# Optimization experiments

Hardware: AMD Instinct MI355X
Metric: run time of the kernel (lower is better)

The kernel has to match this reference:

```python
import jax, jax.numpy as jnp
import numpy as np
from jax import lax

EPS = 1e-08


def setup_inputs() -> dict:
    key = jax.random.key(0)
    k1, k2, k3 = jax.random.split(key, 3)
    b, cin, cout, ks, h, w = 16, 64, 64, 3, 256, 256
    X = jax.random.normal(k1, (b, cin, h, w), dtype=jnp.float32)
    y = jax.random.normal(k2, (b, cin), dtype=jnp.float32)
    weight = jax.random.normal(k3, (cout, cin, ks, ks), dtype=jnp.float32)
    return {"X": X, "y": y, "weight": weight}


def reference(X, y, weight):
    # EqualizedWeight: scale by Kaiming constant c = (cin*k*k)^-0.5 (gain=lr_mul=1)
    cout, cin, ks, _ = weight.shape
    c = (cin * ks * ks) ** (-0.5)
    w0 = weight * c
    # Modulate: per-sample, per-input-channel scaling -> (b, cout, cin, k, k)
    w1 = w0[None] * y[:, None, :, None, None]
    # Demodulate: normalize each (sample, out-filter) to unit L2 norm
    d = lax.rsqrt(jnp.sum(w1 * w1, axis=(2, 3, 4), keepdims=True) + EPS)
    w1 = w1 * d
    b, _, h, w = X.shape
    # Grouped conv: fold batch into channels, one group per sample
    Xr = X.reshape(1, b * cin, h, w)
    ker = w1.reshape(b * cout, cin, ks, ks)
    out = lax.conv_general_dilated(
        Xr, ker,
        window_strides=(1, 1),
        padding="SAME",
        feature_group_count=b,
        dimension_numbers=("NCHW", "OIHW", "NCHW"),
    )
    return out.reshape(b, cout, h, w)
```

## Files before the change

kernel.cpp:

```cpp
#include <hip/hip_runtime.h>
#include <hip/hip_bf16.h>

typedef __bf16 bf16x8 __attribute__((ext_vector_type(8)));
typedef float  f32x4  __attribute__((ext_vector_type(4)));

#define B_   16
#define CIN  64
#define COUT 64
#define H_   256
#define W_   256
#define TY   16
#define SLOT (258 * 64)

__global__ void modw_kernel(const float* __restrict__ weight,
                            const float* __restrict__ y,
                            __bf16* __restrict__ w1g) {
  const int co = blockIdx.x;
  const int b  = blockIdx.y;
  const int ci = threadIdx.x;
  const float c  = 0.041666666666666664f;
  const float yv = y[b*CIN + ci] * c;
  float w[9];
  float s = 0.0f;
#pragma unroll
  for (int t = 0; t < 9; ++t) {
    float wv = weight[(co*CIN + ci)*9 + t] * yv;
    w[t] = wv;
    s += wv * wv;
  }
#pragma unroll
  for (int off = 32; off > 0; off >>= 1) s += __shfl_xor(s, off, 64);
  const float d = rsqrtf(s + 1e-8f);
#pragma unroll
  for (int t = 0; t < 9; ++t)
    w1g[((b*9 + t)*COUT + co)*CIN + ci] = (__bf16)(w[t] * d);
}

__device__ __forceinline__ void stage_load(const float* __restrict__ X,
                                           int b, int yy, int tid, float4* f) {
  const int cg = tid >> 6;
  const int px_base = 4 * (tid & 63);
  const float* xrow = X + ((long)b * (CIN * H_ * W_) + (long)yy * W_);
#pragma unroll
  for (int j = 0; j < 8; ++j)
    f[j] = *reinterpret_cast<const float4*>(xrow + (long)(cg * 8 + j) * (H_ * W_) + px_base);
}

__device__ __forceinline__ void stage_write(__bf16* __restrict__ xs, int slot,
                                            int tid, const float4* f, bool valid) {
  const int cg = tid >> 6;
  const int px_base = 4 * (tid & 63);
  bf16x8 frag[4];
  if (valid) {
#pragma unroll
    for (int j = 0; j < 8; ++j) {
      frag[0][j] = (__bf16)f[j].x;
      frag[1][j] = (__bf16)f[j].y;
      frag[2][j] = (__bf16)f[j].z;
      frag[3][j] = (__bf16)f[j].w;
    }
  } else {
#pragma unroll
    for (int o = 0; o < 4; ++o)
#pragma unroll
      for (int j = 0; j < 8; ++j) frag[o][j] = (__bf16)0.f;
  }
#pragma unroll
  for (int oo = 0; oo < 4; ++oo) {
    const int o  = (oo + tid) & 3;
    const int pl = px_base + o + 1;
    const int gs = cg ^ (pl & 7);
    *reinterpret_cast<bf16x8*>(&xs[slot * SLOT + pl * 64 + gs * 8]) = frag[o];
  }
}

__global__ __launch_bounds__(512)
void conv_kernel(const float* __restrict__ X,
                 const __bf16* __restrict__ w1g,
                 float* __restrict__ out) {
  const int y0   = blockIdx.x * TY;
  const int b    = blockIdx.y;
  const int tid  = threadIdx.x;
  const int lane = tid & 63;
  const int wv   = tid >> 6;
  const int cgw  = wv & 1;
  const int pg   = wv >> 1;
  const int q    = lane >> 4;
  const int n    = lane & 15;

  __shared__ __bf16 xs[3 * SLOT];

  if (tid < 384) {
    const int s = tid >> 7, r = tid & 127;
    const int col = (r < 64) ? 0 : 257;
    xs[s * SLOT + col * 64 + (r & 63)] = (__bf16)0.f;
  }

  {
    float4 f[8];
#pragma unroll
    for (int k = 0; k < 3; ++k) {
      const int yy = y0 - 1 + k;
      const bool valid = (yy >= 0);
      if (valid) stage_load(X, b, yy, tid, f);
      stage_write(xs, (yy + 3) % 3, tid, f, valid);
    }
  }

  float4 pf[8];
  for (int ty = 0; ty < TY; ++ty) {
    const int y = y0 + ty;
    __syncthreads();

    const int yy = y + 2;
    const bool do_pf = (ty < TY - 1);
    const bool pf_ok = do_pf && (yy < H_);
    if (pf_ok) stage_load(X, b, yy, tid, pf);

    f32x4 acc[2][4];
#pragma unroll
    for (int c2 = 0; c2 < 2; ++c2)
#pragma unroll
      for (int nt = 0; nt < 4; ++nt) acc[c2][nt] = (f32x4){0.f, 0.f, 0.f, 0.f};

#pragma unroll
    for (int dy = 0; dy < 3; ++dy) {
      const __bf16* sl = &xs[((y - 1 + dy + 3) % 3) * SLOT];

      bf16x8 afr[2][3][2];
#pragma unroll
      for (int c2 = 0; c2 < 2; ++c2) {
        const int co = cgw * 32 + c2 * 16 + n;
#pragma unroll
        for (int dx = 0; dx < 3; ++dx) {
          const int tap = dy * 3 + dx;
          const __bf16* wp = w1g + ((b * 9 + tap) * COUT + co) * CIN + q * 8;
          afr[c2][dx][0] = *reinterpret_cast<const bf16x8*>(wp);
          afr[c2][dx][1] = *reinterpret_cast<const bf16x8*>(wp + 32);
        }
      }

#pragma unroll
      for (int dx = 0; dx < 3; ++dx) {
        const int p3 = (n + dx) & 7;
        const int o0 = (q ^ p3) * 8;
        const int o1 = ((q + 4) ^ p3) * 8;
#pragma unroll
        for (int nt = 0; nt < 4; ++nt) {
          const int px = pg * 64 + nt * 16 + n + dx;
          const bf16x8 b0 = *reinterpret_cast<const bf16x8*>(&sl[px * 64 + o0]);
          const bf16x8 b1 = *reinterpret_cast<const bf16x8*>(&sl[px * 64 + o1]);
          acc[0][nt] = __builtin_amdgcn_mfma_f32_16x16x32_bf16(afr[0][dx][0], b0, acc[0][nt], 0, 0, 0);
          acc[0][nt] = __builtin_amdgcn_mfma_f32_16x16x32_bf16(afr[0][dx][1], b1, acc[0][nt], 0, 0, 0);
          acc[1][nt] = __builtin_amdgcn_mfma_f32_16x16x32_bf16(afr[1][dx][0], b0, acc[1][nt], 0, 0, 0);
          acc[1][nt] = __builtin_amdgcn_mfma_f32_16x16x32_bf16(afr[1][dx][1], b1, acc[1][nt], 0, 0, 0);
        }
      }
    }
    __syncthreads();

#pragma unroll
    for (int c2 = 0; c2 < 2; ++c2) {
#pragma unroll
      for (int r = 0; r < 4; ++r) {
        const int co = cgw * 32 + c2 * 16 + q * 4 + r;
        float* op = out + ((long)(b * COUT + co) * H_ + y) * W_ + pg * 64 + n;
#pragma unroll
        for (int nt = 0; nt < 4; ++nt) op[nt * 16] = acc[c2][nt][r];
      }
    }

    if (do_pf) stage_write(xs, yy % 3, tid, pf, pf_ok);
  }
}

extern "C" void kernel_launch(void* const* d_in, const int* in_sizes, int n_in,
                              void* d_out, int out_size, void* d_ws, size_t ws_size,
                              hipStream_t stream) {
  const float* X = (const float*)d_in[0];
  const float* y = (const float*)d_in[1];
  const float* w = (const float*)d_in[2];
  float* outp = (float*)d_out;
  __bf16* w1g = (__bf16*)d_ws;

  modw_kernel<<<dim3(COUT, B_), 64, 0, stream>>>(w, y, w1g);
  conv_kernel<<<dim3(H_ / TY, B_), 512, 0, stream>>>(X, w1g, outp);
}
```

Baseline: 625.0 us.

## Hoist modulated weights into registers and swap MFMA operands for float4 stores

Loads all nine taps of modulated weight fragments into registers once per block instead of reloading them from global memory for every output row and dy. Swaps the MFMA A/B operands so each lane's accumulator covers four consecutive pixels, which lets the output be written as float4 vector stores instead of scalar stores. Adds a launch_bounds minimum of two blocks per SM, which caps register use while the weight fragments add about 144 VGPRs, so spilling is a risk.

```diff
diff --git a/kernel.cpp b/kernel.cpp
--- a/kernel.cpp
+++ b/kernel.cpp
@@ -74,7 +74,7 @@
   }
 }
 
-__global__ __launch_bounds__(512)
+__global__ __launch_bounds__(512, 2)
 void conv_kernel(const float* __restrict__ X,
                  const __bf16* __restrict__ w1g,
                  float* __restrict__ out) {
@@ -94,6 +94,18 @@
     const int s = tid >> 7, r = tid & 127;
     const int col = (r < 64) ? 0 : 257;
     xs[s * SLOT + col * 64 + (r & 63)] = (__bf16)0.f;
+  }
+
+  bf16x8 wfr[2][9][2];
+#pragma unroll
+  for (int c2 = 0; c2 < 2; ++c2) {
+    const int co = cgw * 32 + c2 * 16 + n;
+#pragma unroll
+    for (int tap = 0; tap < 9; ++tap) {
+      const __bf16* wp = w1g + ((b * 9 + tap) * COUT + co) * CIN + q * 8;
+      wfr[c2][tap][0] = *reinterpret_cast<const bf16x8*>(wp);
+      wfr[c2][tap][1] = *reinterpret_cast<const bf16x8*>(wp + 32);
+    }
   }
 
   {
@@ -126,34 +138,21 @@
 #pragma unroll
     for (int dy = 0; dy < 3; ++dy) {
       const __bf16* sl = &xs[((y - 1 + dy + 3) % 3) * SLOT];
-
-      bf16x8 afr[2][3][2];
-#pragma unroll
-      for (int c2 = 0; c2 < 2; ++c2) {
-        const int co = cgw * 32 + c2 * 16 + n;
-#pragma unroll
-        for (int dx = 0; dx < 3; ++dx) {
-          const int tap = dy * 3 + dx;
-          const __bf16* wp = w1g + ((b * 9 + tap) * COUT + co) * CIN + q * 8;
-          afr[c2][dx][0] = *reinterpret_cast<const bf16x8*>(wp);
-          afr[c2][dx][1] = *reinterpret_cast<const bf16x8*>(wp + 32);
-        }
-      }
-
 #pragma unroll
       for (int dx = 0; dx < 3; ++dx) {
+        const int tap = dy * 3 + dx;
         const int p3 = (n + dx) & 7;
         const int o0 = (q ^ p3) * 8;
         const int o1 = ((q + 4) ^ p3) * 8;
 #pragma unroll
         for (int nt = 0; nt < 4; ++nt) {
           const int px = pg * 64 + nt * 16 + n + dx;
-          const bf16x8 b0 = *reinterpret_cast<const bf16x8*>(&sl[px * 64 + o0]);
-          const bf16x8 b1 = *reinterpret_cast<const bf16x8*>(&sl[px * 64 + o1]);
-          acc[0][nt] = __builtin_amdgcn_mfma_f32_16x16x32_bf16(afr[0][dx][0], b0, acc[0][nt], 0, 0, 0);
-          acc[0][nt] = __builtin_amdgcn_mfma_f32_16x16x32_bf16(afr[0][dx][1], b1, acc[0][nt], 0, 0, 0);
-          acc[1][nt] = __builtin_amdgcn_mfma_f32_16x16x32_bf16(afr[1][dx][0], b0, acc[1][nt], 0, 0, 0);
-          acc[1][nt] = __builtin_amdgcn_mfma_f32_16x16x32_bf16(afr[1][dx][1], b1, acc[1][nt], 0, 0, 0);
+          const bf16x8 a0 = *reinterpret_cast<const bf16x8*>(&sl[px * 64 + o0]);
+          const bf16x8 a1 = *reinterpret_cast<const bf16x8*>(&sl[px * 64 + o1]);
+          acc[0][nt] = __builtin_amdgcn_mfma_f32_16x16x32_bf16(a0, wfr[0][tap][0], acc[0][nt], 0, 0, 0);
+          acc[0][nt] = __builtin_amdgcn_mfma_f32_16x16x32_bf16(a1, wfr[0][tap][1], acc[0][nt], 0, 0, 0);
+          acc[1][nt] = __builtin_amdgcn_mfma_f32_16x16x32_bf16(a0, wfr[1][tap][0], acc[1][nt], 0, 0, 0);
+          acc[1][nt] = __builtin_amdgcn_mfma_f32_16x16x32_bf16(a1, wfr[1][tap][1], acc[1][nt], 0, 0, 0);
         }
       }
     }
@@ -161,12 +160,12 @@
 
 #pragma unroll
     for (int c2 = 0; c2 < 2; ++c2) {
+      const int co = cgw * 32 + c2 * 16 + n;
 #pragma unroll
-      for (int r = 0; r < 4; ++r) {
-        const int co = cgw * 32 + c2 * 16 + q * 4 + r;
-        float* op = out + ((long)(b * COUT + co) * H_ + y) * W_ + pg * 64 + n;
-#pragma unroll
-        for (int nt = 0; nt < 4; ++nt) op[nt * 16] = acc[c2][nt][r];
+      for (int nt = 0; nt < 4; ++nt) {
+        const int px0 = pg * 64 + nt * 16 + q * 4;
+        *reinterpret_cast<float4*>(out + ((long)(b * COUT + co) * H_ + y) * W_ + px0) =
+            *reinterpret_cast<const float4*>(&acc[c2][nt]);
       }
     }
 
```

Measured after the change: 606.1 us. 1.03x faster.
